# Optimization experiments

Hardware: AMD Instinct MI355X
Metric: run time of the kernel (lower is better)

Reference implementation:

```python
import jax, jax.numpy as jnp
from jax import lax
import numpy as np

B, N, NPOINT, NSAMPLE = 16, 4096, 1024, 32
RADIUS = 0.2
D_FEAT = 64
IN_CH = 3 + D_FEAT
MLP = (64, 64, 128)
EPS = 1e-5


def fps(xyz, npoint):
    # farthest point sampling, xyz: [B,N,3] -> idx [B,npoint] (start at index 0)
    Bn, Nn, _ = xyz.shape
    batch = jnp.arange(Bn)

    def step(carry, _):
        dist, far = carry                      # dist [B,N], far [B]
        centroid = xyz[batch, far]             # [B,3]
        d = jnp.sum((xyz - centroid[:, None, :]) ** 2, -1)
        dist = jnp.minimum(dist, d)
        new_far = jnp.argmax(dist, -1).astype(jnp.int32)
        return (dist, new_far), far

    init = (jnp.full((Bn, Nn), 1e10, xyz.dtype), jnp.zeros((Bn,), jnp.int32))
    _, idxs = lax.scan(step, init, None, length=npoint)
    return jnp.transpose(idxs)                 # [B, npoint]


def square_distance(a, b):
    # a [B,S,3], b [B,N,3] -> [B,S,N]
    return (jnp.sum(a * a, -1)[:, :, None]
            + jnp.sum(b * b, -1)[:, None, :]
            - 2.0 * jnp.einsum('bsc,bnc->bsn', a, b))


def query_ball(radius, nsample, xyz, new_xyz):
    Nn = xyz.shape[1]
    sqr = square_distance(new_xyz, xyz)                      # [B,S,N]
    gi = jnp.where(sqr > radius ** 2, Nn, jnp.arange(Nn, dtype=jnp.int32))
    gi = jnp.sort(gi, axis=-1)[:, :, :nsample]               # [B,S,K]
    first = gi[:, :, :1]
    return jnp.where(gi == Nn, first, gi)


def gather_points(pts, idx):
    # pts [B,N,C], idx [B,...] -> [B,...,C]
    return jax.vmap(lambda p, i: p[i])(pts, idx)


def _forward(xyz, points, params):
    x = jnp.transpose(xyz, (0, 2, 1))          # [B,N,3]
    p = jnp.transpose(points, (0, 2, 1))       # [B,N,D]
    fidx = fps(x, NPOINT)                      # [B,S]
    new_xyz = gather_points(x, fidx)           # [B,S,3]
    idx = query_ball(RADIUS, NSAMPLE, x, new_xyz)  # [B,S,K]
    g_xyz = gather_points(x, idx)              # [B,S,K,3]
    g_norm = g_xyz - new_xyz[:, :, None, :]
    g_pts = gather_points(p, idx)              # [B,S,K,D]
    feat = jnp.concatenate([g_norm, g_pts], -1)  # [B,S,K,3+D]
    h = jnp.transpose(feat, (0, 3, 2, 1))      # [B,C,K,S]
    for (w, b, g, bt) in params:
        h = jnp.einsum('bcks,oc->boks', h, w) + b[None, :, None, None]
        m = jnp.mean(h, axis=(0, 2, 3), keepdims=True)
        v = jnp.mean((h - m) ** 2, axis=(0, 2, 3), keepdims=True)  # biased var (train BN)
        h = g[None, :, None, None] * (h - m) * lax.rsqrt(v + EPS) + bt[None, :, None, None]
        h = jax.nn.relu(h)
    new_points = jnp.max(h, axis=2)            # [B,Cout,S]
    return jnp.transpose(new_xyz, (0, 2, 1)), new_points


def setup_inputs() -> dict:
    key = jax.random.key(0)
    ks = jax.random.split(key, 16)
    xyz = jax.random.uniform(ks[0], (B, 3, N), dtype=jnp.float32)
    points = jax.random.normal(ks[1], (B, D_FEAT, N), dtype=jnp.float32)
    inp = {'xyz': xyz, 'points': points}
    cin = IN_CH
    for l, cout in enumerate(MLP):
        scale = 1.0 / np.sqrt(cin)
        inp[f'w{l}'] = jax.random.normal(ks[2 + 4 * l], (cout, cin), dtype=jnp.float32) * scale
        inp[f'b{l}'] = jax.random.normal(ks[3 + 4 * l], (cout,), dtype=jnp.float32) * scale
        inp[f'g{l}'] = jnp.ones((cout,), jnp.float32)
        inp[f'bt{l}'] = jnp.zeros((cout,), jnp.float32)
        cin = cout
    return inp


def reference(xyz, points, w0, b0, g0, bt0, w1, b1, g1, bt1, w2, b2, g2, bt2):
    params = [(w0, b0, g0, bt0), (w1, b1, g1, bt1), (w2, b2, g2, bt2)]
    return _forward(xyz, points, params)
```

## Files before the change

### kernel.cpp

```cpp
#include <hip/hip_runtime.h>
#include <stdint.h>

#define NB    16
#define NN    4096
#define NP    1024
#define NS    32
#define NGRP  (NB*NP)
#define CNT   524288.0

typedef short  bf16x8 __attribute__((ext_vector_type(8)));
typedef float  f32x4  __attribute__((ext_vector_type(4)));

__device__ __forceinline__ float bf2f(unsigned short u) {
    return __uint_as_float(((unsigned)u) << 16);
}
__device__ __forceinline__ unsigned short f2bf(float f) {
    unsigned u = __float_as_uint(f);
    unsigned r = u + 0x7fffu + ((u >> 16) & 1u);
    return (unsigned short)(r >> 16);
}
__device__ __forceinline__ bf16x8 as_bf(uint4 u) {
    union { uint4 a; bf16x8 b; } c; c.a = u; return c.b;
}

template <int CTRL, int RM>
__device__ __forceinline__ unsigned long long dppmax(unsigned long long k) {
    int lo = (int)(unsigned)k;
    int hi = (int)(k >> 32);
    int ml = __builtin_amdgcn_update_dpp(lo, lo, CTRL, RM, 0xf, false);
    int mh = __builtin_amdgcn_update_dpp(hi, hi, CTRL, RM, 0xf, false);
    unsigned long long m = ((unsigned long long)(unsigned)mh << 32) | (unsigned)ml;
    return m > k ? m : k;
}

__global__ __launch_bounds__(256, 1) void fps_t_kernel(const float* __restrict__ xyz,
                                                       const float* __restrict__ points,
                                                       const float* __restrict__ w0,
                                                       int* __restrict__ fidx,
                                                       unsigned short* __restrict__ T) {
    if (blockIdx.x >= 16) {
        int gid = (blockIdx.x - 16) * 256 + threadIdx.x;
        int b = gid >> 12, n = gid & (NN - 1);
        const float* xb = xyz + (size_t)b * 3 * NN;
        const float* pb = points + (size_t)b * 64 * NN;
        float acc[64];
#pragma unroll
        for (int o = 0; o < 64; o++) acc[o] = 0.f;
        for (int c = 0; c < 67; c++) {
            float v = (c < 3) ? xb[c * NN + n] : pb[(c - 3) * NN + n];
#pragma unroll
            for (int o = 0; o < 64; o++) acc[o] = fmaf(v, w0[o * 67 + c], acc[o]);
        }
        unsigned short* dst = T + (size_t)gid * 64;
        for (int oo = 0; oo < 64; oo += 8) {
            union { unsigned short u[8]; uint4 v; } r;
#pragma unroll
            for (int j = 0; j < 8; j++) r.u[j] = f2bf(acc[oo + j]);
            *(uint4*)&dst[oo] = r.v;
        }
        return;
    }
    int b = blockIdx.x, tid = threadIdx.x;
    const float* xb = xyz + (size_t)b * 3 * NN;
    __shared__ float4 sxyz4[NN];
    __shared__ unsigned long long red[2][4];
    __shared__ int fbuf[NP];
    float px[16], py[16], pz[16], dist[16];
#pragma unroll
    for (int i = 0; i < 16; i++) {
        int n = i * 256 + tid;
        px[i] = xb[n]; py[i] = xb[NN + n]; pz[i] = xb[2 * NN + n];
        sxyz4[n] = make_float4(px[i], py[i], pz[i], 0.f);
        dist[i] = 1e10f;
    }
#pragma unroll
    for (int i = 0; i < 16; i++) {
        asm volatile("" : "+v"(px[i]));
        asm volatile("" : "+v"(py[i]));
        asm volatile("" : "+v"(pz[i]));
    }
    int wv = tid >> 6;
    if (tid == 0) fbuf[0] = 0;
    int far = 0;
    __syncthreads();
    for (int t = 0; t < NP; t++) {
        float4 c = sxyz4[far];
        float cx = c.x, cy = c.y, cz = c.z;
        float tv[16]; int ti[16];
#pragma unroll
        for (int i = 0; i < 16; i++) {
            float dx = __fsub_rn(px[i], cx);
            float dy = __fsub_rn(py[i], cy);
            float dz = __fsub_rn(pz[i], cz);
            float d = __fadd_rn(__fadd_rn(__fmul_rn(dx, dx), __fmul_rn(dy, dy)),
                                __fmul_rn(dz, dz));
            float nd = fminf(dist[i], d);
            dist[i] = nd;
            tv[i] = nd; ti[i] = i;
        }
#pragma unroll
        for (int s = 1; s < 16; s <<= 1) {
#pragma unroll
            for (int i = 0; i < 16; i += 2 * s) {
                if (tv[i + s] > tv[i]) { tv[i] = tv[i + s]; ti[i] = ti[i + s]; }
            }
        }
        int n_best = ti[0] * 256 + tid;
        unsigned long long k =
            ((unsigned long long)__float_as_uint(tv[0]) << 32) |
            (unsigned long long)(~(unsigned)n_best);
        k = dppmax<0x111, 0xf>(k);
        k = dppmax<0x112, 0xf>(k);
        k = dppmax<0x114, 0xf>(k);
        k = dppmax<0x118, 0xf>(k);
        k = dppmax<0x142, 0xa>(k);
        k = dppmax<0x143, 0xc>(k);
        if ((tid & 63) == 63) red[t & 1][wv] = k;
        __syncthreads();
        ulonglong2 ra = *(ulonglong2*)&red[t & 1][0];
        ulonglong2 rb = *(ulonglong2*)&red[t & 1][2];
        unsigned long long r0 = ra.x, r1 = ra.y, r2 = rb.x, r3 = rb.y;
        if (r1 > r0) r0 = r1;
        if (r3 > r2) r2 = r3;
        if (r2 > r0) r0 = r2;
        far = (int)(~(unsigned)r0);
        if (tid == 0 && t + 1 < NP) fbuf[t + 1] = far;
    }
    __syncthreads();
    for (int i = tid; i < NP; i += 256) fidx[b * NP + i] = fbuf[i];
}

__global__ __launch_bounds__(256) void group_kernel(const float* __restrict__ xyz,
                                                    const unsigned short* __restrict__ T,
                                                    const int* __restrict__ fidx,
                                                    int* __restrict__ idx,
                                                    const float* __restrict__ w0,
                                                    const float* __restrict__ b0,
                                                    double* __restrict__ stage1,
                                                    float* __restrict__ out0) {
    __shared__ int gidx[4][NS];
    int t = threadIdx.x, wv = t >> 6, lane = t & 63;
    int g = blockIdx.x * 4 + wv;
    int b = g >> 10, s = g & 1023;
    const float* xb = xyz + (size_t)b * 3 * NN;
    int fid = fidx[g];
    float cx = xb[fid], cy = xb[NN + fid], cz = xb[2 * NN + fid];
    if (lane < 3) {
        float v = (lane == 0) ? cx : ((lane == 1) ? cy : cz);
        out0[((size_t)b * 3 + lane) * NP + s] = v;
    }
    float sa = __fadd_rn(__fadd_rn(__fmul_rn(cx, cx), __fmul_rn(cy, cy)),
                         __fmul_rn(cz, cz));
    int* out = idx + (size_t)g * NS;
    int total = 0; int first = 0;
    for (int ci = 0; ci < NN / 64; ci++) {
        int n = ci * 64 + lane;
        float x = xb[n], y = xb[NN + n], z = xb[2 * NN + n];
        float sb = __fadd_rn(__fadd_rn(__fmul_rn(x, x), __fmul_rn(y, y)),
                             __fmul_rn(z, z));
        float dot = __fadd_rn(__fadd_rn(__fmul_rn(x, cx), __fmul_rn(y, cy)),
                              __fmul_rn(z, cz));
        float sqr = __fsub_rn(__fadd_rn(sa, sb), __fmul_rn(2.0f, dot));
        bool pred = !(sqr > 0.04f);
        unsigned long long mask = __ballot(pred);
        if (mask) {
            if (total == 0) first = ci * 64 + (int)__builtin_ctzll(mask);
            int pos = total + (int)__popcll(mask & ((1ull << lane) - 1ull));
            if (pred && pos < NS) { out[pos] = n; gidx[wv][pos] = n; }
            total += (int)__popcll(mask);
            if (total >= NS) break;
        }
    }
    if (total < NS) {
        if (lane >= total && lane < NS) { out[lane] = first; gidx[wv][lane] = first; }
    }
    int o = lane;
    float uo = fmaf(w0[o * 67 + 2], cz, fmaf(w0[o * 67 + 1], cy, w0[o * 67] * cx));
    float bo = b0[o];
    const unsigned short* Tb = T + (size_t)b * NN * 64;
    float s1 = 0.f, s2 = 0.f;
    for (int k = 0; k < NS; k++) {
        int n = gidx[wv][k];
        float tv = bf2f(Tb[(size_t)n * 64 + o]);
        float h = tv - uo + bo;
        s1 += h; s2 = fmaf(h, h, s2);
    }
    int slot = g & 63;
    atomicAdd(&stage1[slot * 128 + o], (double)s1);
    atomicAdd(&stage1[slot * 128 + 64 + o], (double)s2);
}

__global__ void finalize_kernel(const double* __restrict__ stage, int C,
                                const float* __restrict__ gamma,
                                const float* __restrict__ beta,
                                float* __restrict__ AB) {
    int o = threadIdx.x;
    double s = 0.0, q = 0.0;
    for (int i = 0; i < 64; i++) {
        s += stage[i * 2 * C + o];
        q += stage[i * 2 * C + C + o];
    }
    double m = s * (1.0 / CNT);
    double v = q * (1.0 / CNT) - m * m;
    double A = (double)gamma[o] / sqrt(v + 1e-5);
    AB[o] = (float)A;
    AB[C + o] = (float)((double)beta[o] - m * A);
}

__global__ __launch_bounds__(256) void layer2_kernel(const float* __restrict__ xyz,
                                                     const unsigned short* __restrict__ T,
                                                     const int* __restrict__ fidx,
                                                     const int* __restrict__ idx,
                                                     const float* __restrict__ w0,
                                                     const float* __restrict__ b0,
                                                     const float* __restrict__ AB1,
                                                     const float* __restrict__ w1,
                                                     const float* __restrict__ b1,
                                                     unsigned short* __restrict__ h2,
                                                     double* __restrict__ stage2) {
    __shared__ __attribute__((aligned(16))) unsigned short w1s[64][72];
    __shared__ __attribute__((aligned(16))) unsigned short h1s[4][32][72];
    __shared__ float psum[64], psq[64];
    int t = threadIdx.x, wv = t >> 6, lane = t & 63;
    int quad = lane >> 4, col = lane & 15;
    int g = blockIdx.x * 4 + wv;
    int b = g >> 10;
    for (int lin = t; lin < 4096; lin += 256)
        w1s[lin >> 6][lin & 63] = f2bf(w1[lin]);
    if (t < 64) { psum[t] = 0.f; psq[t] = 0.f; }
    {
        int fid = fidx[g];
        const float* xb = xyz + (size_t)b * 3 * NN;
        float cx = xb[fid], cy = xb[NN + fid], cz = xb[2 * NN + fid];
        int o = lane;
        float uo = fmaf(w0[o * 67 + 2], cz, fmaf(w0[o * 67 + 1], cy, w0[o * 67] * cx));
        float bo = b0[o];
        float a1 = AB1[o], bb1 = AB1[64 + o];
        const int* gi = idx + (size_t)g * NS;
        const unsigned short* Tb = T + (size_t)b * NN * 64;
        for (int k = 0; k < NS; k++) {
            int n = gi[k];
            float tv = bf2f(Tb[(size_t)n * 64 + o]);
            float h = tv - uo + bo;
            float hn = fmaxf(fmaf(h, a1, bb1), 0.f);
            h1s[wv][k][o] = f2bf(hn);
        }
    }
    __syncthreads();
    f32x4 acc[2][4];
#pragma unroll
    for (int i = 0; i < 2; i++)
#pragma unroll
        for (int j = 0; j < 4; j++) acc[i][j] = (f32x4){0.f, 0.f, 0.f, 0.f};
#pragma unroll
    for (int ks = 0; ks < 2; ks++) {
        bf16x8 a0 = as_bf(*(const uint4*)&h1s[wv][col][ks * 32 + quad * 8]);
        bf16x8 a1f = as_bf(*(const uint4*)&h1s[wv][16 + col][ks * 32 + quad * 8]);
#pragma unroll
        for (int nt = 0; nt < 4; nt++) {
            bf16x8 bf = as_bf(*(const uint4*)&w1s[nt * 16 + col][ks * 32 + quad * 8]);
            acc[0][nt] = __builtin_amdgcn_mfma_f32_16x16x32_bf16(a0, bf, acc[0][nt], 0, 0, 0);
            acc[1][nt] = __builtin_amdgcn_mfma_f32_16x16x32_bf16(a1f, bf, acc[1][nt], 0, 0, 0);
        }
    }
    float s1[4], s2[4];
#pragma unroll
    for (int nt = 0; nt < 4; nt++) {
        float bb = b1[nt * 16 + col];
        s1[nt] = 0.f; s2[nt] = 0.f;
#pragma unroll
        for (int mt = 0; mt < 2; mt++)
#pragma unroll
            for (int r = 0; r < 4; r++) {
                float v = acc[mt][nt][r] + bb;
                s1[nt] += v; s2[nt] = fmaf(v, v, s2[nt]);
                h1s[wv][mt * 16 + quad * 4 + r][nt * 16 + col] = f2bf(v);
            }
        s1[nt] += __shfl_xor(s1[nt], 16); s1[nt] += __shfl_xor(s1[nt], 32);
        s2[nt] += __shfl_xor(s2[nt], 16); s2[nt] += __shfl_xor(s2[nt], 32);
        if (quad == 0) {
            atomicAdd(&psum[nt * 16 + col], s1[nt]);
            atomicAdd(&psq[nt * 16 + col], s2[nt]);
        }
    }
#pragma unroll
    for (int r = 0; r < 4; r++) {
        int lin = lane + 64 * r;
        int row = lin >> 3, c = lin & 7;
        uint4 v = *(const uint4*)&h1s[wv][row][c * 8];
        *(uint4*)&h2[((size_t)g * NS + row) * 64 + c * 8] = v;
    }
    __syncthreads();
    if (t < 64) {
        int slot = blockIdx.x & 63;
        atomicAdd(&stage2[slot * 128 + t], (double)psum[t]);
        atomicAdd(&stage2[slot * 128 + 64 + t], (double)psq[t]);
    }
}

__global__ __launch_bounds__(256) void layer3_kernel(const unsigned short* __restrict__ h2,
                                                     const float* __restrict__ AB2,
                                                     const float* __restrict__ w2,
                                                     const float* __restrict__ b2,
                                                     double* __restrict__ stage3,
                                                     float* __restrict__ mxbuf,
                                                     float* __restrict__ mnbuf) {
    __shared__ __attribute__((aligned(16))) unsigned short w2s[128][72];
    __shared__ __attribute__((aligned(16))) unsigned short h2s[4][32][72];
    __shared__ float psum[128], psq[128];
    int t = threadIdx.x, wv = t >> 6, lane = t & 63;
    int quad = lane >> 4, col = lane & 15;
    int g = blockIdx.x * 4 + wv;
    for (int lin = t; lin < 8192; lin += 256)
        w2s[lin >> 6][lin & 63] = f2bf(w2[lin]);
    if (t < 128) { psum[t] = 0.f; psq[t] = 0.f; }
    {
        int c = lane & 7;
        float a2v[8], bb2v[8];
#pragma unroll
        for (int j = 0; j < 8; j++) {
            a2v[j] = AB2[c * 8 + j];
            bb2v[j] = AB2[64 + c * 8 + j];
        }
        const unsigned short* hg = h2 + (size_t)g * NS * 64;
#pragma unroll
        for (int r = 0; r < 4; r++) {
            int row = (lane >> 3) + 8 * r;
            union { uint4 v; unsigned short u[8]; } in, outp;
            in.v = *(const uint4*)&hg[row * 64 + c * 8];
#pragma unroll
            for (int j = 0; j < 8; j++) {
                float f = bf2f(in.u[j]);
                outp.u[j] = f2bf(fmaxf(fmaf(f, a2v[j], bb2v[j]), 0.f));
            }
            *(uint4*)&h2s[wv][row][c * 8] = outp.v;
        }
    }
    __syncthreads();
    f32x4 acc[2][8];
#pragma unroll
    for (int i = 0; i < 2; i++)
#pragma unroll
        for (int j = 0; j < 8; j++) acc[i][j] = (f32x4){0.f, 0.f, 0.f, 0.f};
#pragma unroll
    for (int ks = 0; ks < 2; ks++) {
        bf16x8 a0 = as_bf(*(const uint4*)&h2s[wv][col][ks * 32 + quad * 8]);
        bf16x8 a1f = as_bf(*(const uint4*)&h2s[wv][16 + col][ks * 32 + quad * 8]);
#pragma unroll
        for (int nt = 0; nt < 8; nt++) {
            bf16x8 bf = as_bf(*(const uint4*)&w2s[nt * 16 + col][ks * 32 + quad * 8]);
            acc[0][nt] = __builtin_amdgcn_mfma_f32_16x16x32_bf16(a0, bf, acc[0][nt], 0, 0, 0);
            acc[1][nt] = __builtin_amdgcn_mfma_f32_16x16x32_bf16(a1f, bf, acc[1][nt], 0, 0, 0);
        }
    }
#pragma unroll
    for (int nt = 0; nt < 8; nt++) {
        float bb = b2[nt * 16 + col];
        float s1 = 0.f, s2 = 0.f, mx = -1e30f, mn = 1e30f;
#pragma unroll
        for (int mt = 0; mt < 2; mt++)
#pragma unroll
            for (int r = 0; r < 4; r++) {
                float v = acc[mt][nt][r] + bb;
                s1 += v; s2 = fmaf(v, v, s2);
                mx = fmaxf(mx, v); mn = fminf(mn, v);
            }
        s1 += __shfl_xor(s1, 16); s1 += __shfl_xor(s1, 32);
        s2 += __shfl_xor(s2, 16); s2 += __shfl_xor(s2, 32);
        mx = fmaxf(mx, __shfl_xor(mx, 16)); mx = fmaxf(mx, __shfl_xor(mx, 32));
        mn = fminf(mn, __shfl_xor(mn, 16)); mn = fminf(mn, __shfl_xor(mn, 32));
        if (quad == 0) {
            atomicAdd(&psum[nt * 16 + col], s1);
            atomicAdd(&psq[nt * 16 + col], s2);
            mxbuf[(size_t)g * 128 + nt * 16 + col] = mx;
            mnbuf[(size_t)g * 128 + nt * 16 + col] = mn;
        }
    }
    __syncthreads();
    if (t < 128) {
        int slot = blockIdx.x & 63;
        atomicAdd(&stage3[slot * 256 + t], (double)psum[t]);
        atomicAdd(&stage3[slot * 256 + 128 + t], (double)psq[t]);
    }
}

__global__ __launch_bounds__(256) void epilogue_kernel(const float* __restrict__ mxbuf,
                                                       const float* __restrict__ mnbuf,
                                                       const float* __restrict__ AB3,
                                                       float* __restrict__ out1) {
    __shared__ float tile[32][65];
    int blk = blockIdx.x;
    int b = blk >> 6; int rem = blk & 63;
    int o0 = (rem >> 4) * 32; int s0 = (rem & 15) * 64;
    int t = threadIdx.x;
#pragma unroll
    for (int j = 0; j < 8; j++) {
        int lin = t + 256 * j;
        int sl = lin >> 5, ol = lin & 31;
        int o = o0 + ol;
        float a = AB3[o], bb = AB3[128 + o];
        size_t src = ((size_t)b * NP + s0 + sl) * 128 + o;
        float v = (a >= 0.f) ? mxbuf[src] : mnbuf[src];
        tile[ol][sl] = fmaxf(fmaf(v, a, bb), 0.f);
    }
    __syncthreads();
#pragma unroll
    for (int j = 0; j < 8; j++) {
        int lin = t + 256 * j;
        int ol = lin >> 6, sl = lin & 63;
        out1[((size_t)b * 128 + o0 + ol) * NP + s0 + sl] = tile[ol][sl];
    }
}

extern "C" void kernel_launch(void* const* d_in, const int* in_sizes, int n_in,
                              void* d_out, int out_size, void* d_ws, size_t ws_size,
                              hipStream_t stream) {
    const float* xyz    = (const float*)d_in[0];
    const float* points = (const float*)d_in[1];
    const float* w0  = (const float*)d_in[2];
    const float* b0  = (const float*)d_in[3];
    const float* g0  = (const float*)d_in[4];
    const float* bt0 = (const float*)d_in[5];
    const float* w1  = (const float*)d_in[6];
    const float* b1  = (const float*)d_in[7];
    const float* g1  = (const float*)d_in[8];
    const float* bt1 = (const float*)d_in[9];
    const float* w2  = (const float*)d_in[10];
    const float* b2  = (const float*)d_in[11];
    const float* g2  = (const float*)d_in[12];
    const float* bt2 = (const float*)d_in[13];

    char* ws = (char*)d_ws;
    int*            fidx = (int*)(ws + 0);
    int*            idx  = (int*)(ws + 65536);
    unsigned short* T    = (unsigned short*)(ws + 2162688);
    unsigned short* h2   = (unsigned short*)(ws + 10551296);
    float*          mxbuf = (float*)(ws + 77660160);
    float*          mnbuf = (float*)(ws + 86048768);
    double*         stage = (double*)(ws + 94437376);
    float*          AB   = (float*)(ws + 94699520);
    double* stage1 = stage;
    double* stage2 = stage + 64 * 128;
    double* stage3 = stage + 2 * 64 * 128;
    float* AB1 = AB; float* AB2 = AB + 128; float* AB3 = AB + 256;
    float* out0 = (float*)d_out;
    float* out1 = out0 + NB * 3 * NP;

    hipMemsetAsync(stage, 0, 64 * 512 * 8, stream);

    fps_t_kernel<<<16 + 256, 256, 0, stream>>>(xyz, points, w0, fidx, T);
    group_kernel<<<NGRP / 4, 256, 0, stream>>>(xyz, T, fidx, idx, w0, b0, stage1, out0);
    finalize_kernel<<<1, 64, 0, stream>>>(stage1, 64, g0, bt0, AB1);
    layer2_kernel<<<NGRP / 4, 256, 0, stream>>>(xyz, T, fidx, idx, w0, b0, AB1,
                                                w1, b1, h2, stage2);
    finalize_kernel<<<1, 64, 0, stream>>>(stage2, 64, g1, bt1, AB2);
    layer3_kernel<<<NGRP / 4, 256, 0, stream>>>(h2, AB2, w2, b2, stage3, mxbuf, mnbuf);
    finalize_kernel<<<1, 128, 0, stream>>>(stage3, 128, g2, bt2, AB3);
    epilogue_kernel<<<1024, 256, 0, stream>>>(mxbuf, mnbuf, AB3, out1);
}
```

Before: 894.3 us.

## Shorten FPS critical path, fuse BN finalize into layers, cap FPS grid

```diff
diff --git a/kernel.cpp b/kernel.cpp
--- a/kernel.cpp
+++ b/kernel.cpp
@@ -39,31 +39,34 @@
                                                        int* __restrict__ fidx,
                                                        unsigned short* __restrict__ T) {
     if (blockIdx.x >= 16) {
-        int gid = (blockIdx.x - 16) * 256 + threadIdx.x;
-        int b = gid >> 12, n = gid & (NN - 1);
-        const float* xb = xyz + (size_t)b * 3 * NN;
-        const float* pb = points + (size_t)b * 64 * NN;
-        float acc[64];
-#pragma unroll
-        for (int o = 0; o < 64; o++) acc[o] = 0.f;
-        for (int c = 0; c < 67; c++) {
-            float v = (c < 3) ? xb[c * NN + n] : pb[(c - 3) * NN + n];
-#pragma unroll
-            for (int o = 0; o < 64; o++) acc[o] = fmaf(v, w0[o * 67 + c], acc[o]);
-        }
-        unsigned short* dst = T + (size_t)gid * 64;
-        for (int oo = 0; oo < 64; oo += 8) {
-            union { unsigned short u[8]; uint4 v; } r;
-#pragma unroll
-            for (int j = 0; j < 8; j++) r.u[j] = f2bf(acc[oo + j]);
-            *(uint4*)&dst[oo] = r.v;
+        for (int chunk = blockIdx.x - 16; chunk < 256; chunk += 240) {
+            int gid = chunk * 256 + threadIdx.x;
+            int b = gid >> 12, n = gid & (NN - 1);
+            const float* xb = xyz + (size_t)b * 3 * NN;
+            const float* pb = points + (size_t)b * 64 * NN;
+            float acc[64];
+#pragma unroll
+            for (int o = 0; o < 64; o++) acc[o] = 0.f;
+            for (int c = 0; c < 67; c++) {
+                float v = (c < 3) ? xb[c * NN + n] : pb[(c - 3) * NN + n];
+#pragma unroll
+                for (int o = 0; o < 64; o++) acc[o] = fmaf(v, w0[o * 67 + c], acc[o]);
+            }
+            unsigned short* dst = T + (size_t)gid * 64;
+            for (int oo = 0; oo < 64; oo += 8) {
+                union { unsigned short u[8]; uint4 v; } r;
+#pragma unroll
+                for (int j = 0; j < 8; j++) r.u[j] = f2bf(acc[oo + j]);
+                *(uint4*)&dst[oo] = r.v;
+            }
         }
         return;
     }
     int b = blockIdx.x, tid = threadIdx.x;
     const float* xb = xyz + (size_t)b * 3 * NN;
     __shared__ float4 sxyz4[NN];
-    __shared__ unsigned long long red[2][4];
+    __shared__ unsigned long long redk[2][4];
+    __shared__ float4 redc[2][4];
     __shared__ int fbuf[NP];
     float px[16], py[16], pz[16], dist[16];
 #pragma unroll
@@ -80,12 +83,24 @@
         asm volatile("" : "+v"(pz[i]));
     }
     int wv = tid >> 6;
-    if (tid == 0) fbuf[0] = 0;
-    int far = 0;
+    if (tid == 0) {
+        redk[0][0] = ~0ull; redk[0][1] = 0ull; redk[0][2] = 0ull; redk[0][3] = 0ull;
+        redc[0][0] = make_float4(px[0], py[0], pz[0], 0.f);
+    }
     __syncthreads();
     for (int t = 0; t < NP; t++) {
-        float4 c = sxyz4[far];
-        float cx = c.x, cy = c.y, cz = c.z;
+        int p = t & 1;
+        ulonglong2 ka = *(ulonglong2*)&redk[p][0];
+        ulonglong2 kb = *(ulonglong2*)&redk[p][2];
+        float4 c0 = redc[p][0], c1 = redc[p][1];
+        float4 c2 = redc[p][2], c3 = redc[p][3];
+        unsigned long long k0 = ka.x, k1 = ka.y, k2 = kb.x, k3 = kb.y;
+        if (k1 > k0) { k0 = k1; c0 = c1; }
+        if (k3 > k2) { k2 = k3; c2 = c3; }
+        if (k2 > k0) { k0 = k2; c0 = c2; }
+        int far = (int)(~(unsigned)k0);
+        if (tid == 0) fbuf[t] = far;
+        float cx = c0.x, cy = c0.y, cz = c0.z;
         float tv[16]; int ti[16];
 #pragma unroll
         for (int i = 0; i < 16; i++) {
@@ -115,18 +130,13 @@
         k = dppmax<0x118, 0xf>(k);
         k = dppmax<0x142, 0xa>(k);
         k = dppmax<0x143, 0xc>(k);
-        if ((tid & 63) == 63) red[t & 1][wv] = k;
+        if ((tid & 63) == 63) {
+            int nwin = (int)(~(unsigned)k);
+            redk[p ^ 1][wv] = k;
+            redc[p ^ 1][wv] = sxyz4[nwin];
+        }
         __syncthreads();
-        ulonglong2 ra = *(ulonglong2*)&red[t & 1][0];
-        ulonglong2 rb = *(ulonglong2*)&red[t & 1][2];
-        unsigned long long r0 = ra.x, r1 = ra.y, r2 = rb.x, r3 = rb.y;
-        if (r1 > r0) r0 = r1;
-        if (r3 > r2) r2 = r3;
-        if (r2 > r0) r0 = r2;
-        far = (int)(~(unsigned)r0);
-        if (tid == 0 && t + 1 < NP) fbuf[t + 1] = far;
-    }
-    __syncthreads();
+    }
     for (int i = tid; i < NP; i += 256) fidx[b * NP + i] = fbuf[i];
 }
 
@@ -137,8 +147,13 @@
                                                     const float* __restrict__ w0,
                                                     const float* __restrict__ b0,
                                                     double* __restrict__ stage1,
-                                                    float* __restrict__ out0) {
+                                                    float* __restrict__ out0,
+                                                    const float* __restrict__ gamma,
+                                                    const float* __restrict__ beta,
+                                                    float* __restrict__ AB,
+                                                    unsigned* __restrict__ ctr) {
     __shared__ int gidx[4][NS];
+    __shared__ int lastf;
     int t = threadIdx.x, wv = t >> 6, lane = t & 63;
     int g = blockIdx.x * 4 + wv;
     int b = g >> 10, s = g & 1023;
@@ -188,23 +203,27 @@
     int slot = g & 63;
     atomicAdd(&stage1[slot * 128 + o], (double)s1);
     atomicAdd(&stage1[slot * 128 + 64 + o], (double)s2);
-}
-
-__global__ void finalize_kernel(const double* __restrict__ stage, int C,
-                                const float* __restrict__ gamma,
-                                const float* __restrict__ beta,
-                                float* __restrict__ AB) {
-    int o = threadIdx.x;
-    double s = 0.0, q = 0.0;
-    for (int i = 0; i < 64; i++) {
-        s += stage[i * 2 * C + o];
-        q += stage[i * 2 * C + C + o];
-    }
-    double m = s * (1.0 / CNT);
-    double v = q * (1.0 / CNT) - m * m;
-    double A = (double)gamma[o] / sqrt(v + 1e-5);
-    AB[o] = (float)A;
-    AB[C + o] = (float)((double)beta[o] - m * A);
+    __syncthreads();
+    if (t == 0) {
+        unsigned prev = __hip_atomic_fetch_add(ctr, 1u, __ATOMIC_ACQ_REL,
+                                               __HIP_MEMORY_SCOPE_AGENT);
+        lastf = (prev == (unsigned)(NGRP / 4 - 1));
+    }
+    __syncthreads();
+    if (lastf && t < 64) {
+        double ss = 0.0, q = 0.0;
+        for (int i = 0; i < 64; i++) {
+            ss += __hip_atomic_load(&stage1[i * 128 + t], __ATOMIC_RELAXED,
+                                    __HIP_MEMORY_SCOPE_AGENT);
+            q  += __hip_atomic_load(&stage1[i * 128 + 64 + t], __ATOMIC_RELAXED,
+                                    __HIP_MEMORY_SCOPE_AGENT);
+        }
+        double m = ss * (1.0 / CNT);
+        double v = q * (1.0 / CNT) - m * m;
+        double A = (double)gamma[t] / sqrt(v + 1e-5);
+        AB[t] = (float)A;
+        AB[64 + t] = (float)((double)beta[t] - m * A);
+    }
 }
 
 __global__ __launch_bounds__(256) void layer2_kernel(const float* __restrict__ xyz,
@@ -217,10 +236,15 @@
                                                      const float* __restrict__ w1,
                                                      const float* __restrict__ b1,
                                                      unsigned short* __restrict__ h2,
-                                                     double* __restrict__ stage2) {
+                                                     double* __restrict__ stage2,
+                                                     const float* __restrict__ gamma,
+                                                     const float* __restrict__ beta,
+                                                     float* __restrict__ AB2out,
+                                                     unsigned* __restrict__ ctr) {
     __shared__ __attribute__((aligned(16))) unsigned short w1s[64][72];
     __shared__ __attribute__((aligned(16))) unsigned short h1s[4][32][72];
     __shared__ float psum[64], psq[64];
+    __shared__ int lastf;
     int t = threadIdx.x, wv = t >> 6, lane = t & 63;
     int quad = lane >> 4, col = lane & 15;
     int g = blockIdx.x * 4 + wv;
@@ -296,6 +320,27 @@
         atomicAdd(&stage2[slot * 128 + t], (double)psum[t]);
         atomicAdd(&stage2[slot * 128 + 64 + t], (double)psq[t]);
     }
+    __syncthreads();
+    if (t == 0) {
+        unsigned prev = __hip_atomic_fetch_add(ctr, 1u, __ATOMIC_ACQ_REL,
+                                               __HIP_MEMORY_SCOPE_AGENT);
+        lastf = (prev == (unsigned)(NGRP / 4 - 1));
+    }
+    __syncthreads();
+    if (lastf && t < 64) {
+        double ss = 0.0, q = 0.0;
+        for (int i = 0; i < 64; i++) {
+            ss += __hip_atomic_load(&stage2[i * 128 + t], __ATOMIC_RELAXED,
+                                    __HIP_MEMORY_SCOPE_AGENT);
+            q  += __hip_atomic_load(&stage2[i * 128 + 64 + t], __ATOMIC_RELAXED,
+                                    __HIP_MEMORY_SCOPE_AGENT);
+        }
+        double m = ss * (1.0 / CNT);
+        double v = q * (1.0 / CNT) - m * m;
+        double A = (double)gamma[t] / sqrt(v + 1e-5);
+        AB2out[t] = (float)A;
+        AB2out[64 + t] = (float)((double)beta[t] - m * A);
+    }
 }
 
 __global__ __launch_bounds__(256) void layer3_kernel(const unsigned short* __restrict__ h2,
@@ -304,10 +349,15 @@
                                                      const float* __restrict__ b2,
                                                      double* __restrict__ stage3,
                                                      float* __restrict__ mxbuf,
-                                                     float* __restrict__ mnbuf) {
+                                                     float* __restrict__ mnbuf,
+                                                     const float* __restrict__ gamma,
+                                                     const float* __restrict__ beta,
+                                                     float* __restrict__ AB3out,
+                                                     unsigned* __restrict__ ctr) {
     __shared__ __attribute__((aligned(16))) unsigned short w2s[128][72];
     __shared__ __attribute__((aligned(16))) unsigned short h2s[4][32][72];
     __shared__ float psum[128], psq[128];
+    __shared__ int lastf;
     int t = threadIdx.x, wv = t >> 6, lane = t & 63;
     int quad = lane >> 4, col = lane & 15;
     int g = blockIdx.x * 4 + wv;
@@ -381,6 +431,27 @@
         int slot = blockIdx.x & 63;
         atomicAdd(&stage3[slot * 256 + t], (double)psum[t]);
         atomicAdd(&stage3[slot * 256 + 128 + t], (double)psq[t]);
+    }
+    __syncthreads();
+    if (t == 0) {
+        unsigned prev = __hip_atomic_fetch_add(ctr, 1u, __ATOMIC_ACQ_REL,
+                                               __HIP_MEMORY_SCOPE_AGENT);
+        lastf = (prev == (unsigned)(NGRP / 4 - 1));
+    }
+    __syncthreads();
+    if (lastf && t < 128) {
+        double ss = 0.0, q = 0.0;
+        for (int i = 0; i < 64; i++) {
+            ss += __hip_atomic_load(&stage3[i * 256 + t], __ATOMIC_RELAXED,
+                                    __HIP_MEMORY_SCOPE_AGENT);
+            q  += __hip_atomic_load(&stage3[i * 256 + 128 + t], __ATOMIC_RELAXED,
+                                    __HIP_MEMORY_SCOPE_AGENT);
+        }
+        double m = ss * (1.0 / CNT);
+        double v = q * (1.0 / CNT) - m * m;
+        double A = (double)gamma[t] / sqrt(v + 1e-5);
+        AB3out[t] = (float)A;
+        AB3out[128 + t] = (float)((double)beta[t] - m * A);
     }
 }
 
@@ -438,7 +509,8 @@
     float*          mxbuf = (float*)(ws + 77660160);
     float*          mnbuf = (float*)(ws + 86048768);
     double*         stage = (double*)(ws + 94437376);
-    float*          AB   = (float*)(ws + 94699520);
+    unsigned*       ctrs  = (unsigned*)(ws + 94437376 + 262144);
+    float*          AB   = (float*)(ws + 94437376 + 262400);
     double* stage1 = stage;
     double* stage2 = stage + 64 * 128;
     double* stage3 = stage + 2 * 64 * 128;
@@ -446,15 +518,15 @@
     float* out0 = (float*)d_out;
     float* out1 = out0 + NB * 3 * NP;
 
-    hipMemsetAsync(stage, 0, 64 * 512 * 8, stream);
-
-    fps_t_kernel<<<16 + 256, 256, 0, stream>>>(xyz, points, w0, fidx, T);
-    group_kernel<<<NGRP / 4, 256, 0, stream>>>(xyz, T, fidx, idx, w0, b0, stage1, out0);
-    finalize_kernel<<<1, 64, 0, stream>>>(stage1, 64, g0, bt0, AB1);
+    hipMemsetAsync(stage, 0, 262144 + 256, stream);
+
+    fps_t_kernel<<<256, 256, 0, stream>>>(xyz, points, w0, fidx, T);
+    group_kernel<<<NGRP / 4, 256, 0, stream>>>(xyz, T, fidx, idx, w0, b0, stage1,
+                                               out0, g0, bt0, AB1, ctrs + 0);
     layer2_kernel<<<NGRP / 4, 256, 0, stream>>>(xyz, T, fidx, idx, w0, b0, AB1,
-                                                w1, b1, h2, stage2);
-    finalize_kernel<<<1, 64, 0, stream>>>(stage2, 64, g1, bt1, AB2);
-    layer3_kernel<<<NGRP / 4, 256, 0, stream>>>(h2, AB2, w2, b2, stage3, mxbuf, mnbuf);
-    finalize_kernel<<<1, 128, 0, stream>>>(stage3, 128, g2, bt2, AB3);
+                                                w1, b1, h2, stage2,
+                                                g1, bt1, AB2, ctrs + 1);
+    layer3_kernel<<<NGRP / 4, 256, 0, stream>>>(h2, AB2, w2, b2, stage3, mxbuf, mnbuf,
+                                                g2, bt2, AB3, ctrs + 2);
     epilogue_kernel<<<1024, 256, 0, stream>>>(mxbuf, mnbuf, AB3, out1);
 }
```

Measured after the change: 1.243 ms. +39.0%, slower.
